# Optimization experiments

Hardware: AMD Instinct MI355X
Metric: run time of the kernel (lower is better)

Reference implementation:

```python
import jax, jax.numpy as jnp
import numpy as np

NUM_HEADS = 8
KEY_DIM = 16
D = 32          # attn_ratio * key_dim
DH = D * NUM_HEADS  # 256
NH_KD = KEY_DIM * NUM_HEADS  # 128
DIM = 256


def _conv1x1_bn(x, W, s, b):
    # 1x1 conv (no bias) followed by eval-mode BatchNorm folded to affine.
    # x: [B, Cin, H, W], W: [Cout, Cin], s/b: [Cout]
    y = jnp.einsum('oc,bchw->bohw', W, x)
    return y * s[None, :, None, None] + b[None, :, None, None]


def setup_inputs() -> dict:
    key = jax.random.key(0)
    ks = jax.random.split(key, 16)
    B, C, H, Wd = 2, DIM, 64, 64
    rgb = jax.random.normal(ks[0], (B, C, H, Wd), dtype=jnp.float32)
    edge = jax.random.normal(ks[1], (B, C, H, Wd), dtype=jnp.float32)

    def conv_w(k, o, i):
        return jax.random.normal(k, (o, i), dtype=jnp.float32) * (1.0 / np.sqrt(i))

    def bn(k, c):
        k1, k2 = jax.random.split(k)
        s = jax.random.uniform(k1, (c,), dtype=jnp.float32, minval=0.5, maxval=1.5)
        b = jax.random.normal(k2, (c,), dtype=jnp.float32) * 0.1
        return s, b

    Wq = conv_w(ks[2], NH_KD, C); sq, bq = bn(ks[3], NH_KD)
    Wk = conv_w(ks[4], NH_KD, C); sk, bk = bn(ks[5], NH_KD)
    Wv = conv_w(ks[6], DH, C);   sv, bv = bn(ks[7], DH)
    Wp = conv_w(ks[8], C, DH);   sp, bp = bn(ks[9], C)
    return dict(rgb=rgb, edge=edge, Wq=Wq, sq=sq, bq=bq, Wk=Wk, sk=sk, bk=bk,
                Wv=Wv, sv=sv, bv=bv, Wp=Wp, sp=sp, bp=bp)


def reference(rgb, edge, Wq, sq, bq, Wk, sk, bk, Wv, sv, bv, Wp, sp, bp):
    B, C, H, Wd = rgb.shape
    N = H * Wd
    # Q from rgb, K/V from edge (all 1x1 conv + BN)
    qq = _conv1x1_bn(rgb, Wq, sq, bq).reshape(B, NUM_HEADS, KEY_DIM, N)
    qq = jnp.transpose(qq, (0, 1, 3, 2))                       # [B,h,N,kd]
    kk = _conv1x1_bn(edge, Wk, sk, bk).reshape(B, NUM_HEADS, KEY_DIM, N)  # [B,h,kd,N]
    vv = _conv1x1_bn(edge, Wv, sv, bv).reshape(B, NUM_HEADS, D, N)
    vv = jnp.transpose(vv, (0, 1, 3, 2))                       # [B,h,N,d]
    # NOTE: original forward does NOT apply self.scale -- faithful omission.
    attn = jnp.einsum('bhnk,bhkm->bhnm', qq, kk)               # [B,h,N,N]
    attn = jax.nn.softmax(attn, axis=-1)
    xx = jnp.einsum('bhnm,bhmd->bhnd', attn, vv)               # [B,h,N,d]
    xx = jnp.transpose(xx, (0, 1, 3, 2)).reshape(B, DH, H, Wd)
    xx = jax.nn.relu(xx)                                       # activation before proj conv
    xx = _conv1x1_bn(xx, Wp, sp, bp)                           # [B,C,H,W]
    return xx
```

## Files before the change

### kernel.cpp

```cpp
#include <hip/hip_runtime.h>
#include <hip/hip_bf16.h>

#define NB 2
#define CIN 256
#define NPIX 4096
#define NHEADS 8
#define KD 16
#define DV 32
#define DH 256
#define NHKD 128

typedef short bf16x8 __attribute__((ext_vector_type(8)));
typedef short s16x4 __attribute__((ext_vector_type(4)));
typedef float f32x2 __attribute__((ext_vector_type(2)));
typedef float f32x4 __attribute__((ext_vector_type(4)));
typedef float f32x16 __attribute__((ext_vector_type(16)));
typedef unsigned int u32x2 __attribute__((ext_vector_type(2)));
typedef unsigned int u32x4 __attribute__((ext_vector_type(4)));

#define LOG2E 1.4426950408889634f

static __device__ __forceinline__ unsigned short f2bf(float f) {
    __hip_bfloat16 h = __float2bfloat16(f);
    return __builtin_bit_cast(unsigned short, h);
}

static __device__ __forceinline__ unsigned pack_rhu(float lo, float hi) {
    unsigned a = __builtin_bit_cast(unsigned, lo) + 0x8000u;
    unsigned b = __builtin_bit_cast(unsigned, hi) + 0x8000u;
    return (a >> 16) | (b & 0xffff0000u);
}

__global__ __launch_bounds__(256) void k_prep(
    const float* __restrict__ Wq, const float* __restrict__ Wk,
    const float* __restrict__ Wv, const float* __restrict__ Wp,
    unsigned short* __restrict__ wq, unsigned short* __restrict__ wk,
    unsigned short* __restrict__ wv, unsigned short* __restrict__ wp)
{
    int i = blockIdx.x * 256 + threadIdx.x;
    if (i < NHKD * CIN) { wq[i] = f2bf(Wq[i]); wk[i] = f2bf(Wk[i]); }
    if (i < DH * CIN)   { wv[i] = f2bf(Wv[i]); wp[i] = f2bf(Wp[i]); }
}

__global__ __launch_bounds__(256) void k_qkv(
    const float* __restrict__ rgb, const float* __restrict__ edge,
    const unsigned short* __restrict__ wq, const unsigned short* __restrict__ wk,
    const unsigned short* __restrict__ wv,
    const float* __restrict__ sq, const float* __restrict__ bq,
    const float* __restrict__ sk, const float* __restrict__ bk,
    const float* __restrict__ sv, const float* __restrict__ bv,
    unsigned short* __restrict__ Qw, unsigned short* __restrict__ Kw,
    unsigned short* __restrict__ Vw)
{
    const int nb = blockIdx.x;
    const int ob = blockIdx.y;
    const int b  = blockIdx.z;
    const int tid = threadIdx.x;
    const int wave = tid >> 6, lane = tid & 63;
    const int cl = lane & 15, g = lane >> 4;

    const float* X; const unsigned short* W; const float* sc; const float* bi;
    int obase, job;
    if (ob < 2)      { X = rgb  + (size_t)b*CIN*NPIX; W = wq; sc = sq; bi = bq; obase = ob*64;     job = 0; }
    else if (ob < 4) { X = edge + (size_t)b*CIN*NPIX; W = wk; sc = sk; bi = bk; obase = (ob-2)*64; job = 1; }
    else             { X = edge + (size_t)b*CIN*NPIX; W = wv; sc = sv; bi = bv; obase = (ob-4)*64; job = 2; }

    __shared__ float xt[32 * 65];

    f32x4 acc[4];
    #pragma unroll
    for (int i = 0; i < 4; i++) acc[i] = (f32x4)0.f;

    const int n0 = nb * 64;
    const int ow = obase + wave * 16 + cl;
    const unsigned short* Wrow = W + (size_t)ow * CIN;

    for (int kt = 0; kt < 8; kt++) {
        __syncthreads();
        {
            int tr = tid >> 6;
            int tc = tid & 63;
            #pragma unroll
            for (int r = 0; r < 8; r++) {
                int c_local = r * 4 + tr;
                xt[c_local * 65 + tc] = X[(size_t)(kt * 32 + c_local) * NPIX + n0 + tc];
            }
        }
        __syncthreads();
        #pragma unroll
        for (int ns = 0; ns < 4; ns++) {
            u32x4 aw;
            #pragma unroll
            for (int w = 0; w < 4; w++)
                aw[w] = pack_rhu(xt[(8 * g + 2 * w) * 65 + ns * 16 + cl],
                                 xt[(8 * g + 2 * w + 1) * 65 + ns * 16 + cl]);
            bf16x8 a = __builtin_bit_cast(bf16x8, aw);
            bf16x8 wfrag = *reinterpret_cast<const bf16x8*>(Wrow + kt * 32 + 8 * g);
            acc[ns] = __builtin_amdgcn_mfma_f32_16x16x32_bf16(a, wfrag, acc[ns], 0, 0, 0);
        }
    }

    const float sco = sc[ow], bio = bi[ow];
    if (job == 2) {
        int h = ow >> 5, d = ow & 31;
        unsigned short* dst = Vw + ((size_t)((b * 8 + h) * 32 + d)) * NPIX;
        #pragma unroll
        for (int ns = 0; ns < 4; ns++) {
            int nr = n0 + ns * 16 + 4 * g;
            s16x4 pk;
            #pragma unroll
            for (int r = 0; r < 4; r++) pk[r] = (short)f2bf(acc[ns][r] * sco + bio);
            *reinterpret_cast<s16x4*>(dst + nr) = pk;
        }
    } else {
        float scq = sco, biq = bio;
        if (job == 0) { scq *= LOG2E; biq *= LOG2E; }
        unsigned short* base = (job == 0) ? Qw : Kw;
        int h = ow >> 4, kd = ow & 15;
        unsigned short* dst = base + ((size_t)(b * 8 + h) * NPIX) * KD + kd;
        #pragma unroll
        for (int ns = 0; ns < 4; ns++)
            #pragma unroll
            for (int r = 0; r < 4; r++) {
                int nr = n0 + ns * 16 + 4 * g + r;
                dst[(size_t)nr * KD] = f2bf(acc[ns][r] * scq + biq);
            }
    }
}

typedef const unsigned int __attribute__((address_space(1)))* gp_t;
typedef unsigned int __attribute__((address_space(3)))* lp_t;

__global__ __launch_bounds__(256, 4) void k_attn(
    const unsigned short* __restrict__ Qw, const unsigned short* __restrict__ Kw,
    const unsigned short* __restrict__ Vw, unsigned short* __restrict__ Ow)
{
    const int qg = blockIdx.x;
    const int bh = blockIdx.y;
    const int tid = threadIdx.x;
    const int wave = tid >> 6, lane = tid & 63;
    const int l31 = lane & 31, hi = lane >> 5;

    __shared__ union {
        unsigned short v[4][2048];
        struct { float o[4][32][32]; float l[4][32]; } c;
    } sh;

    const unsigned short* Kbase = Kw + (size_t)bh * NPIX * KD;
    const unsigned short* Vbase = Vw + (size_t)bh * DV * NPIX;

    const int q0 = qg * 32;
    const bf16x8 qf = *(const bf16x8*)(Qw + ((size_t)bh * NPIX + q0 + l31) * KD + 8 * hi);

    const unsigned short* Kln = Kbase + (size_t)l31 * KD + 8 * hi;
#define KF0(T) (*(const bf16x8*)(Kln + ((T) * 64 + 0) * KD))
#define KF1(T) (*(const bf16x8*)(Kln + ((T) * 64 + 32) * KD))

    const int scb = ((lane & 7) * 16) ^ ((lane >> 3) << 4);
    const unsigned short* Vln = Vbase + (size_t)(lane >> 3) * NPIX + (scb >> 1);
#define STAGE(T) do { _Pragma("unroll") for (int j = 0; j < 4; ++j) \
    __builtin_amdgcn_global_load_lds( \
        (gp_t)(const void*)(Vln + (size_t)j * 8 * NPIX + (size_t)(T) * 64), \
        (lp_t)(void*)(&sh.v[wave][j * 512]), 16, 0, 0); } while (0)

    const int vsw = (l31 & 7) << 4;

    f32x16 o = (f32x16)0.f;
    float l_run = 0.f;
    const f32x16 z16 = (f32x16)0.f;

    const int T0 = wave * 16;

    #pragma unroll
    for (int t = 0; t < 16; ++t) {
        const int T = T0 + t;
        bf16x8 ka0 = KF0(T);
        bf16x8 ka1 = KF1(T);
        asm volatile("s_waitcnt lgkmcnt(0)" ::: "memory");
        STAGE(T);

        __builtin_amdgcn_s_setprio(1);
        f32x16 s0 = __builtin_amdgcn_mfma_f32_32x32x16_bf16(ka0, qf, z16, 0, 0, 0);
        __builtin_amdgcn_s_setprio(0);
        #pragma unroll
        for (int i = 0; i < 16; ++i) s0[i] = __builtin_amdgcn_exp2f(s0[i]);
        {
            f32x2 p[4];
            #pragma unroll
            for (int j = 0; j < 4; ++j) {
                f32x2 a = {s0[2*j], s0[2*j+1]};
                f32x2 b = {s0[2*j+8], s0[2*j+9]};
                p[j] = a + b;
            }
            p[0] += p[2]; p[1] += p[3]; p[0] += p[1];
            l_run += p[0].x + p[0].y;
        }
        unsigned u0[8];
        #pragma unroll
        for (int ss = 0; ss < 8; ++ss) u0[ss] = pack_rhu(s0[2*ss], s0[2*ss+1]);
        #pragma unroll
        for (int gg = 0; gg < 2; ++gg) {
            u32x2 r0 = __builtin_amdgcn_permlane32_swap(u0[4*gg+0], u0[4*gg+2], false, false);
            u0[4*gg+0] = r0.x; u0[4*gg+2] = r0.y;
            u32x2 r1 = __builtin_amdgcn_permlane32_swap(u0[4*gg+1], u0[4*gg+3], false, false);
            u0[4*gg+1] = r1.x; u0[4*gg+3] = r1.y;
        }

        __builtin_amdgcn_s_setprio(1);
        f32x16 s1 = __builtin_amdgcn_mfma_f32_32x32x16_bf16(ka1, qf, z16, 0, 0, 0);
        __builtin_amdgcn_s_setprio(0);
        asm volatile("s_waitcnt vmcnt(0)" ::: "memory");

        __builtin_amdgcn_s_setprio(1);
        {
            u32x4 av;
            av.x = u0[0]; av.y = u0[1]; av.z = u0[2]; av.w = u0[3];
            const int vi0 = (l31 * 128 + ((16 * hi) ^ vsw)) >> 1;
            bf16x8 vb0 = *(const bf16x8*)(&sh.v[wave][vi0]);
            o = __builtin_amdgcn_mfma_f32_32x32x16_bf16(__builtin_bit_cast(bf16x8, av), vb0, o, 0, 0, 0);
            av.x = u0[4]; av.y = u0[5]; av.z = u0[6]; av.w = u0[7];
            const int vi1 = (l31 * 128 + ((32 + 16 * hi) ^ vsw)) >> 1;
            bf16x8 vb1 = *(const bf16x8*)(&sh.v[wave][vi1]);
            o = __builtin_amdgcn_mfma_f32_32x32x16_bf16(__builtin_bit_cast(bf16x8, av), vb1, o, 0, 0, 0);
        }
        __builtin_amdgcn_s_setprio(0);

        #pragma unroll
        for (int i = 0; i < 16; ++i) s1[i] = __builtin_amdgcn_exp2f(s1[i]);
        {
            f32x2 p[4];
            #pragma unroll
            for (int j = 0; j < 4; ++j) {
                f32x2 a = {s1[2*j], s1[2*j+1]};
                f32x2 b = {s1[2*j+8], s1[2*j+9]};
                p[j] = a + b;
            }
            p[0] += p[2]; p[1] += p[3]; p[0] += p[1];
            l_run += p[0].x + p[0].y;
        }
        unsigned u1[8];
        #pragma unroll
        for (int ss = 0; ss < 8; ++ss) u1[ss] = pack_rhu(s1[2*ss], s1[2*ss+1]);
        #pragma unroll
        for (int gg = 0; gg < 2; ++gg) {
            u32x2 r0 = __builtin_amdgcn_permlane32_swap(u1[4*gg+0], u1[4*gg+2], false, false);
            u1[4*gg+0] = r0.x; u1[4*gg+2] = r0.y;
            u32x2 r1 = __builtin_amdgcn_permlane32_swap(u1[4*gg+1], u1[4*gg+3], false, false);
            u1[4*gg+1] = r1.x; u1[4*gg+3] = r1.y;
        }

        __builtin_amdgcn_s_setprio(1);
        {
            u32x4 av;
            av.x = u1[0]; av.y = u1[1]; av.z = u1[2]; av.w = u1[3];
            const int vi2 = (l31 * 128 + ((64 + 16 * hi) ^ vsw)) >> 1;
            bf16x8 vb2 = *(const bf16x8*)(&sh.v[wave][vi2]);
            o = __builtin_amdgcn_mfma_f32_32x32x16_bf16(__builtin_bit_cast(bf16x8, av), vb2, o, 0, 0, 0);
            av.x = u1[4]; av.y = u1[5]; av.z = u1[6]; av.w = u1[7];
            const int vi3 = (l31 * 128 + ((96 + 16 * hi) ^ vsw)) >> 1;
            bf16x8 vb3 = *(const bf16x8*)(&sh.v[wave][vi3]);
            o = __builtin_amdgcn_mfma_f32_32x32x16_bf16(__builtin_bit_cast(bf16x8, av), vb3, o, 0, 0, 0);
        }
        __builtin_amdgcn_s_setprio(0);
    }
#undef KF0
#undef KF1
#undef STAGE

    l_run += __shfl_xor(l_run, 32, 64);

    __syncthreads();
    #pragma unroll
    for (int r = 0; r < 16; ++r) {
        const int qr = (r & 3) + 8 * (r >> 2) + 4 * hi;
        sh.c.o[wave][qr][l31] = o[r];
    }
    if (hi == 0) sh.c.l[wave][l31] = l_run;
    __syncthreads();

    const int q = tid >> 3;
    const int d0 = (tid & 7) * 4;
    const float lsum = sh.c.l[0][q] + sh.c.l[1][q] + sh.c.l[2][q] + sh.c.l[3][q];
    const float linv = __builtin_amdgcn_rcpf(lsum);
    float v[4];
    #pragma unroll
    for (int i = 0; i < 4; ++i) {
        float s = sh.c.o[0][q][d0+i] + sh.c.o[1][q][d0+i] + sh.c.o[2][q][d0+i] + sh.c.o[3][q][d0+i];
        v[i] = fmaxf(s * linv, 0.f);
    }
    const int b = bh >> 3, h = bh & 7;
    u32x2 pk;
    pk.x = (unsigned)f2bf(v[0]) | ((unsigned)f2bf(v[1]) << 16);
    pk.y = (unsigned)f2bf(v[2]) | ((unsigned)f2bf(v[3]) << 16);
    *reinterpret_cast<u32x2*>(Ow + ((size_t)b * NPIX + q0 + q) * DH + h * DV + d0) = pk;
}

__global__ __launch_bounds__(256) void k_proj(
    const unsigned short* __restrict__ Xo, const unsigned short* __restrict__ wp,
    const float* __restrict__ sp, const float* __restrict__ bp,
    float* __restrict__ out)
{
    const int nb = blockIdx.x;
    const int b  = blockIdx.y;
    const int tid = threadIdx.x;
    const int wave = tid >> 6, lane = tid & 63;
    const int cl = lane & 15, g = lane >> 4;

    const int cbase = wave * 64;
    f32x4 acc[4][2];
    #pragma unroll
    for (int i = 0; i < 4; i++)
        #pragma unroll
        for (int j = 0; j < 2; j++) acc[i][j] = (f32x4)0.f;

    const unsigned short* Xb = Xo + ((size_t)b * NPIX + nb * 32) * DH;

    #pragma unroll
    for (int kt = 0; kt < 8; kt++) {
        bf16x8 afr[4];
        #pragma unroll
        for (int cs = 0; cs < 4; cs++)
            afr[cs] = *reinterpret_cast<const bf16x8*>(wp + (size_t)(cbase + cs * 16 + cl) * DH + kt * 32 + 8 * g);
        #pragma unroll
        for (int ns = 0; ns < 2; ns++) {
            bf16x8 bfr = *reinterpret_cast<const bf16x8*>(Xb + (size_t)(ns * 16 + cl) * DH + kt * 32 + 8 * g);
            #pragma unroll
            for (int cs = 0; cs < 4; cs++)
                acc[cs][ns] = __builtin_amdgcn_mfma_f32_16x16x32_bf16(afr[cs], bfr, acc[cs][ns], 0, 0, 0);
        }
    }

    #pragma unroll
    for (int cs = 0; cs < 4; cs++)
        #pragma unroll
        for (int r = 0; r < 4; r++) {
            int c = cbase + cs * 16 + 4 * g + r;
            float scv = sp[c], biv = bp[c];
            float* dst = out + ((size_t)b * DH + c) * NPIX + nb * 32;
            #pragma unroll
            for (int ns = 0; ns < 2; ns++)
                dst[ns * 16 + cl] = acc[cs][ns][r] * scv + biv;
        }
}

extern "C" void kernel_launch(void* const* d_in, const int* in_sizes, int n_in,
                              void* d_out, int out_size, void* d_ws, size_t ws_size,
                              hipStream_t stream) {
    const float* rgb  = (const float*)d_in[0];
    const float* edge = (const float*)d_in[1];
    const float* Wq = (const float*)d_in[2];
    const float* sq = (const float*)d_in[3];
    const float* bq = (const float*)d_in[4];
    const float* Wk = (const float*)d_in[5];
    const float* sk = (const float*)d_in[6];
    const float* bk = (const float*)d_in[7];
    const float* Wv = (const float*)d_in[8];
    const float* sv = (const float*)d_in[9];
    const float* bv = (const float*)d_in[10];
    const float* Wp = (const float*)d_in[11];
    const float* sp = (const float*)d_in[12];
    const float* bp = (const float*)d_in[13];
    float* out = (float*)d_out;

    char* ws = (char*)d_ws;
    unsigned short* wq = (unsigned short*)(ws + 0);
    unsigned short* wk = (unsigned short*)(ws + (64 << 10));
    unsigned short* wv = (unsigned short*)(ws + (128 << 10));
    unsigned short* wp = (unsigned short*)(ws + (256 << 10));
    size_t o = 384 << 10;
    unsigned short* Qw = (unsigned short*)(ws + o); o += (size_t)16 * NPIX * KD * 2;
    unsigned short* Kw = (unsigned short*)(ws + o); o += (size_t)16 * NPIX * KD * 2;
    unsigned short* Vw = (unsigned short*)(ws + o); o += (size_t)16 * DV * NPIX * 2;
    unsigned short* Ow = (unsigned short*)(ws + o);

    k_prep<<<dim3(256), dim3(256), 0, stream>>>(Wq, Wk, Wv, Wp, wq, wk, wv, wp);
    k_qkv<<<dim3(64, 8, NB), dim3(256), 0, stream>>>(rgb, edge, wq, wk, wv,
                                                     sq, bq, sk, bk, sv, bv, Qw, Kw, Vw);
    k_attn<<<dim3(128, 16), dim3(256), 0, stream>>>(Qw, Kw, Vw, Ow);
    k_proj<<<dim3(128, NB), dim3(256), 0, stream>>>(Ow, wp, sp, bp, out);
}
```

Before: 87.93 us.

## Permute K row order to drop permlane swaps, pad V LDS rows

The K projection now writes rows in a permuted order within each 16-row group, so the attention score fragment already has the layout the P·V MFMA needs. This removes the permlane32 swaps after softmax packing. Packing now uses the hardware round-to-nearest bf16 conversion instead of manual rounding. The V staging buffer in LDS is padded per 8-row slab to cut bank conflicts, and the final reduction reads vector float4 values. The risk is that the K permutation must match the MFMA output layout exactly, or the results will be wrong.

```diff
diff --git a/kernel.cpp b/kernel.cpp
--- a/kernel.cpp
+++ b/kernel.cpp
@@ -29,6 +29,14 @@
     unsigned a = __builtin_bit_cast(unsigned, lo) + 0x8000u;
     unsigned b = __builtin_bit_cast(unsigned, hi) + 0x8000u;
     return (a >> 16) | (b & 0xffff0000u);
+}
+
+static __device__ __forceinline__ unsigned pack_rn(float lo, float hi) {
+    float2 t; t.x = lo; t.y = hi;
+    __hip_bfloat162 b2 = __float22bfloat162_rn(t);
+    unsigned r;
+    __builtin_memcpy(&r, &b2, 4);
+    return r;
 }
 
 __global__ __launch_bounds__(256) void k_prep(
@@ -115,6 +123,7 @@
     } else {
         float scq = sco, biq = bio;
         if (job == 0) { scq *= LOG2E; biq *= LOG2E; }
+        const int gp = (job == 1) ? (((g & 1) << 1) | (g >> 1)) : g;
         unsigned short* base = (job == 0) ? Qw : Kw;
         int h = ow >> 4, kd = ow & 15;
         unsigned short* dst = base + ((size_t)(b * 8 + h) * NPIX) * KD + kd;
@@ -122,7 +131,7 @@
         for (int ns = 0; ns < 4; ns++)
             #pragma unroll
             for (int r = 0; r < 4; r++) {
-                int nr = n0 + ns * 16 + 4 * g + r;
+                int nr = n0 + ns * 16 + 4 * gp + r;
                 dst[(size_t)nr * KD] = f2bf(acc[ns][r] * scq + biq);
             }
     }
@@ -142,7 +151,7 @@
     const int l31 = lane & 31, hi = lane >> 5;
 
     __shared__ union {
-        unsigned short v[4][2048];
+        unsigned short v[4][2080];
         struct { float o[4][32][32]; float l[4][32]; } c;
     } sh;
 
@@ -161,9 +170,10 @@
 #define STAGE(T) do { _Pragma("unroll") for (int j = 0; j < 4; ++j) \
     __builtin_amdgcn_global_load_lds( \
         (gp_t)(const void*)(Vln + (size_t)j * 8 * NPIX + (size_t)(T) * 64), \
-        (lp_t)(void*)(&sh.v[wave][j * 512]), 16, 0, 0); } while (0)
+        (lp_t)(void*)(&sh.v[wave][j * 520]), 16, 0, 0); } while (0)
 
     const int vsw = (l31 & 7) << 4;
+    const int vbase = (l31 >> 3) * 520 + (l31 & 7) * 64;
 
     f32x16 o = (f32x16)0.f;
     float l_run = 0.f;
@@ -197,14 +207,7 @@
         }
         unsigned u0[8];
         #pragma unroll
-        for (int ss = 0; ss < 8; ++ss) u0[ss] = pack_rhu(s0[2*ss], s0[2*ss+1]);
-        #pragma unroll
-        for (int gg = 0; gg < 2; ++gg) {
-            u32x2 r0 = __builtin_amdgcn_permlane32_swap(u0[4*gg+0], u0[4*gg+2], false, false);
-            u0[4*gg+0] = r0.x; u0[4*gg+2] = r0.y;
-            u32x2 r1 = __builtin_amdgcn_permlane32_swap(u0[4*gg+1], u0[4*gg+3], false, false);
-            u0[4*gg+1] = r1.x; u0[4*gg+3] = r1.y;
-        }
+        for (int ss = 0; ss < 8; ++ss) u0[ss] = pack_rn(s0[2*ss], s0[2*ss+1]);
 
         __builtin_amdgcn_s_setprio(1);
         f32x16 s1 = __builtin_amdgcn_mfma_f32_32x32x16_bf16(ka1, qf, z16, 0, 0, 0);
@@ -215,11 +218,11 @@
         {
             u32x4 av;
             av.x = u0[0]; av.y = u0[1]; av.z = u0[2]; av.w = u0[3];
-            const int vi0 = (l31 * 128 + ((16 * hi) ^ vsw)) >> 1;
+            const int vi0 = vbase + (((16 * hi) ^ vsw) >> 1);
             bf16x8 vb0 = *(const bf16x8*)(&sh.v[wave][vi0]);
             o = __builtin_amdgcn_mfma_f32_32x32x16_bf16(__builtin_bit_cast(bf16x8, av), vb0, o, 0, 0, 0);
             av.x = u0[4]; av.y = u0[5]; av.z = u0[6]; av.w = u0[7];
-            const int vi1 = (l31 * 128 + ((32 + 16 * hi) ^ vsw)) >> 1;
+            const int vi1 = vbase + (((32 + 16 * hi) ^ vsw) >> 1);
             bf16x8 vb1 = *(const bf16x8*)(&sh.v[wave][vi1]);
             o = __builtin_amdgcn_mfma_f32_32x32x16_bf16(__builtin_bit_cast(bf16x8, av), vb1, o, 0, 0, 0);
         }
@@ -240,24 +243,17 @@
         }
         unsigned u1[8];
         #pragma unroll
-        for (int ss = 0; ss < 8; ++ss) u1[ss] = pack_rhu(s1[2*ss], s1[2*ss+1]);
-        #pragma unroll
-        for (int gg = 0; gg < 2; ++gg) {
-            u32x2 r0 = __builtin_amdgcn_permlane32_swap(u1[4*gg+0], u1[4*gg+2], false, false);
-            u1[4*gg+0] = r0.x; u1[4*gg+2] = r0.y;
-            u32x2 r1 = __builtin_amdgcn_permlane32_swap(u1[4*gg+1], u1[4*gg+3], false, false);
-            u1[4*gg+1] = r1.x; u1[4*gg+3] = r1.y;
-        }
+        for (int ss = 0; ss < 8; ++ss) u1[ss] = pack_rn(s1[2*ss], s1[2*ss+1]);
 
         __builtin_amdgcn_s_setprio(1);
         {
             u32x4 av;
             av.x = u1[0]; av.y = u1[1]; av.z = u1[2]; av.w = u1[3];
-            const int vi2 = (l31 * 128 + ((64 + 16 * hi) ^ vsw)) >> 1;
+            const int vi2 = vbase + (((64 + 16 * hi) ^ vsw) >> 1);
             bf16x8 vb2 = *(const bf16x8*)(&sh.v[wave][vi2]);
             o = __builtin_amdgcn_mfma_f32_32x32x16_bf16(__builtin_bit_cast(bf16x8, av), vb2, o, 0, 0, 0);
             av.x = u1[4]; av.y = u1[5]; av.z = u1[6]; av.w = u1[7];
-            const int vi3 = (l31 * 128 + ((96 + 16 * hi) ^ vsw)) >> 1;
+            const int vi3 = vbase + (((96 + 16 * hi) ^ vsw) >> 1);
             bf16x8 vb3 = *(const bf16x8*)(&sh.v[wave][vi3]);
             o = __builtin_amdgcn_mfma_f32_32x32x16_bf16(__builtin_bit_cast(bf16x8, av), vb3, o, 0, 0, 0);
         }
@@ -282,12 +278,13 @@
     const int d0 = (tid & 7) * 4;
     const float lsum = sh.c.l[0][q] + sh.c.l[1][q] + sh.c.l[2][q] + sh.c.l[3][q];
     const float linv = __builtin_amdgcn_rcpf(lsum);
+    f32x4 s4 = *(const f32x4*)(&sh.c.o[0][q][d0]);
+    s4 += *(const f32x4*)(&sh.c.o[1][q][d0]);
+    s4 += *(const f32x4*)(&sh.c.o[2][q][d0]);
+    s4 += *(const f32x4*)(&sh.c.o[3][q][d0]);
     float v[4];
     #pragma unroll
-    for (int i = 0; i < 4; ++i) {
-        float s = sh.c.o[0][q][d0+i] + sh.c.o[1][q][d0+i] + sh.c.o[2][q][d0+i] + sh.c.o[3][q][d0+i];
-        v[i] = fmaxf(s * linv, 0.f);
-    }
+    for (int i = 0; i < 4; ++i) v[i] = fmaxf(s4[i] * linv, 0.f);
     const int b = bh >> 3, h = bh & 7;
     u32x2 pk;
     pk.x = (unsigned)f2bf(v[0]) | ((unsigned)f2bf(v[1]) << 16);
```

Result: faster. 85.45 us (-2.8%).
